# Optimization experiments

Measured on AMD Instinct MI355X. Metric: run time of the kernel, lower is better.

## Reference

```python
import jax
import jax.numpy as jnp
from jax import lax
import numpy as np

TS = 7
DATA_DIM = 1024
HIDDEN = 1024
BATCH = 1024


def setup_inputs() -> dict:
    key = jax.random.key(0)
    ks = jax.random.split(key, 8)
    s = 1.0 / np.sqrt(HIDDEN)
    return {
        "x": jax.random.normal(ks[0], (BATCH, TS, DATA_DIM), dtype=jnp.float32),
        "x_shift": jax.random.normal(ks[1], (BATCH, TS, DATA_DIM), dtype=jnp.float32),
        # PyTorch LSTM params, gate order (i, f, g, o), uniform(-1/sqrt(H), 1/sqrt(H))
        "W_ih": jax.random.uniform(ks[2], (4 * HIDDEN, DATA_DIM), jnp.float32, -s, s),
        "W_hh": jax.random.uniform(ks[3], (4 * HIDDEN, HIDDEN), jnp.float32, -s, s),
        "b_ih": jax.random.uniform(ks[4], (4 * HIDDEN,), jnp.float32, -s, s),
        "b_hh": jax.random.uniform(ks[5], (4 * HIDDEN,), jnp.float32, -s, s),
        "attn_W": jax.random.uniform(ks[6], (1, HIDDEN), jnp.float32, -s, s),
        "attn_b": jax.random.uniform(ks[7], (1,), jnp.float32, -s, s),
    }


def _lstm(x, W_ih, W_hh, b_ih, b_hh):
    # x: [B, T, D] -> h: [B, T, H]; PyTorch gate order i, f, g, o
    B, T, D = x.shape
    H = W_hh.shape[1]
    x_gates = jnp.einsum("btd,gd->btg", x, W_ih) + b_ih + b_hh  # [B, T, 4H]

    def step(carry, xg):
        h, c = carry
        g = xg + h @ W_hh.T  # [B, 4H]
        i, f, gg, o = jnp.split(g, 4, axis=-1)
        i = jax.nn.sigmoid(i)
        f = jax.nn.sigmoid(f)
        gg = jnp.tanh(gg)
        o = jax.nn.sigmoid(o)
        c = f * c + i * gg
        h = o * jnp.tanh(c)
        return (h, c), h

    h0 = jnp.zeros((B, H), x.dtype)
    c0 = jnp.zeros((B, H), x.dtype)
    (_, _), hs = lax.scan(step, (h0, c0), jnp.swapaxes(x_gates, 0, 1))
    return jnp.swapaxes(hs, 0, 1)  # [B, T, H]


def _dam_forward(x, x_shift, W_ih, W_hh, b_ih, b_hh, attn_W, attn_b):
    ts = x.shape[1]
    data_dim = x.shape[2]
    # Temporal covariance: original does bmm -> eye mask -> max(dim=1),
    # which equals relu(diag) since off-diagonal entries become exact zeros.
    t1 = x - x.mean(axis=2, keepdims=True)
    t2 = x_shift - x_shift.mean(axis=2, keepdims=True)
    cov_temp = jnp.maximum(jnp.sum(t1 * t2, axis=2) / ts, 0.0)  # [B, ts]
    # Channel covariance: same trick on [B, data_dim, data_dim] diagonal.
    c1 = x - x.mean(axis=1, keepdims=True)
    c2 = x_shift - x_shift.mean(axis=1, keepdims=True)
    cov_channel = jnp.maximum(jnp.sum(c1 * c2, axis=1) / data_dim, 0.0)  # [B, data_dim]
    # Outer product -> [B, ts, data_dim]
    dist = cov_temp[:, :, None] * cov_channel[:, None, :]
    h = _lstm(dist, W_ih, W_hh, b_ih, b_hh)  # [B, ts, H]
    spatial_attn = jax.nn.softmax(h, axis=1)
    h_tanh = jnp.tanh(h)
    temporal_attn = jax.nn.sigmoid(h_tanh @ attn_W.T + attn_b)  # [B, ts, 1]
    return spatial_attn, temporal_attn


def reference(x, x_shift, W_ih, W_hh, b_ih, b_hh, attn_W, attn_b):
    return _dam_forward(x, x_shift, W_ih, W_hh, b_ih, b_hh, attn_W, attn_b)
```

## Files before the change

kernel.cpp:

```cpp
#include <hip/hip_runtime.h>
#include <math.h>

#define BSZ 1024
#define TS 7
#define DD 1024
#define HH 1024
#define NG 4096

typedef _Float16 f16x8 __attribute__((ext_vector_type(8)));
typedef _Float16 f16x4 __attribute__((ext_vector_type(4)));
typedef float f32x4 __attribute__((ext_vector_type(4)));

__device__ __forceinline__ float sigm_(float x) { return 1.f / (1.f + __expf(-x)); }
__device__ __forceinline__ float tanh_(float x) { return 1.f - 2.f / (__expf(2.f * x) + 1.f); }

__device__ __forceinline__ void gload16(const _Float16* g, _Float16* l) {
  __builtin_amdgcn_global_load_lds(
      (const __attribute__((address_space(1))) void*)g,
      (__attribute__((address_space(3))) void*)l, 16, 0, 0);
}

__global__ __launch_bounds__(256) void conv_w(const float* __restrict__ wih,
                                              const float* __restrict__ whh,
                                              _Float16* __restrict__ o_ih,
                                              _Float16* __restrict__ o_hh) {
  const int N4 = NG * DD / 4;
  for (int i = blockIdx.x * 256 + threadIdx.x; i < 2 * N4;
       i += gridDim.x * 256) {
    const float4 v = (i < N4) ? ((const float4*)wih)[i] : ((const float4*)whh)[i - N4];
    f16x4 o;
    o[0] = (_Float16)v.x; o[1] = (_Float16)v.y;
    o[2] = (_Float16)v.z; o[3] = (_Float16)v.w;
    if (i < N4) ((f16x4*)o_ih)[i] = o;
    else        ((f16x4*)o_hh)[i - N4] = o;
  }
}

__global__ __launch_bounds__(256) void cov_kernel(
    const float* __restrict__ x, const float* __restrict__ xsh,
    float* __restrict__ covT, _Float16* __restrict__ covC16) {
  const int b = blockIdx.x, tid = threadIdx.x;
  const float4* xb = (const float4*)(x + (size_t)b * TS * DD);
  const float4* yb = (const float4*)(xsh + (size_t)b * TS * DD);
  float4 xv[TS], yv[TS];
#pragma unroll
  for (int t = 0; t < TS; t++) {
    xv[t] = xb[t * 256 + tid];
    yv[t] = yb[t * 256 + tid];
  }
  f16x4 cc;
#pragma unroll
  for (int q = 0; q < 4; q++) {
    float sx = 0.f, sy = 0.f, sxy = 0.f;
#pragma unroll
    for (int t = 0; t < TS; t++) {
      float a = ((const float*)&xv[t])[q];
      float c = ((const float*)&yv[t])[q];
      sx += a; sy += c; sxy += a * c;
    }
    float v = (sxy - sx * sy * (1.f / TS)) * (1.f / DD);
    cc[q] = (_Float16)(v > 0.f ? v : 0.f);
  }
  *(f16x4*)&covC16[(size_t)b * DD + tid * 4] = cc;

  float psx[TS], psy[TS], psxy[TS];
#pragma unroll
  for (int t = 0; t < TS; t++) {
    float4 a = xv[t], c = yv[t];
    psx[t] = a.x + a.y + a.z + a.w;
    psy[t] = c.x + c.y + c.z + c.w;
    psxy[t] = a.x * c.x + a.y * c.y + a.z * c.z + a.w * c.w;
  }
#pragma unroll
  for (int t = 0; t < TS; t++) {
    for (int m = 32; m >= 1; m >>= 1) {
      psx[t] += __shfl_xor(psx[t], m);
      psy[t] += __shfl_xor(psy[t], m);
      psxy[t] += __shfl_xor(psxy[t], m);
    }
  }
  __shared__ float red[3][4][TS];
  const int wave = tid >> 6, lane = tid & 63;
  if (lane == 0) {
#pragma unroll
    for (int t = 0; t < TS; t++) {
      red[0][wave][t] = psx[t];
      red[1][wave][t] = psy[t];
      red[2][wave][t] = psxy[t];
    }
  }
  __syncthreads();
  if (tid < TS) {
    float sx = red[0][0][tid] + red[0][1][tid] + red[0][2][tid] + red[0][3][tid];
    float sy = red[1][0][tid] + red[1][1][tid] + red[1][2][tid] + red[1][3][tid];
    float sxy = red[2][0][tid] + red[2][1][tid] + red[2][2][tid] + red[2][3][tid];
    float v = (sxy - sx * sy * (1.f / DD)) * (1.f / TS);
    covT[b * TS + tid] = v > 0.f ? v : 0.f;
  }
}

template <int MODE>
__global__ __launch_bounds__(256) void fused_step(
    const _Float16* __restrict__ A, int lda, const _Float16* __restrict__ W,
    const float* __restrict__ covT, int t, _Float16* __restrict__ M16,
    const float* __restrict__ b_ih, const float* __restrict__ b_hh,
    float* __restrict__ cbuf, _Float16* __restrict__ hout)
{
  __shared__ __align__(16) char smem[49152];
  _Float16* As0 = (_Float16*)smem;
  _Float16* Bs0 = (_Float16*)(smem + 8192);
  _Float16* As1 = (_Float16*)(smem + 24576);
  _Float16* Bs1 = (_Float16*)(smem + 32768);
  float* gls = (float*)smem;

  const int tid = threadIdx.x;
  const int wave = tid >> 6, lane = tid & 63;
  const int l15 = lane & 15, lhi = lane >> 4;
  const int rowBase = blockIdx.y * 64;
  const int jBase = blockIdx.x * 32;
  const int sRow = tid >> 3;
  const int sColSw = (((tid & 7) ^ (sRow & 7)) * 8);
  const int ldsOff = (tid & ~63) * 8;

  f32x4 acc[4][2] = {};

#define STAGE(as, bs, kt)                                                     \
  {                                                                           \
    const int k0 = (kt)*64;                                                   \
    gload16(&A[(size_t)(rowBase + sRow) * lda + k0 + sColSw], (as) + ldsOff); \
    gload16(&A[(size_t)(rowBase + 32 + sRow) * lda + k0 + sColSw],            \
            (as) + 2048 + ldsOff);                                            \
    gload16(&W[(size_t)(0 * HH + jBase + sRow) * DD + k0 + sColSw],           \
            (bs) + 0 + ldsOff);                                               \
    gload16(&W[(size_t)(1 * HH + jBase + sRow) * DD + k0 + sColSw],           \
            (bs) + 2048 + ldsOff);                                            \
    gload16(&W[(size_t)(2 * HH + jBase + sRow) * DD + k0 + sColSw],           \
            (bs) + 4096 + ldsOff);                                            \
    gload16(&W[(size_t)(3 * HH + jBase + sRow) * DD + k0 + sColSw],           \
            (bs) + 6144 + ldsOff);                                            \
  }

#define COMPUTE(as, bs)                                                       \
  {                                                                           \
    _Pragma("unroll") for (int kk = 0; kk < 2; ++kk) {                        \
      const int akx = (kk * 32 + lhi * 8) ^ ((l15 & 7) << 3);                 \
      f16x8 af[4], bf[2];                                                     \
      _Pragma("unroll") for (int mf = 0; mf < 4; ++mf) af[mf] =               \
          *(const f16x8*)&(as)[(mf * 16 + l15) * 64 + akx];                   \
      _Pragma("unroll") for (int nf = 0; nf < 2; ++nf) bf[nf] =               \
          *(const f16x8*)&(bs)[(wave * 32 + nf * 16 + l15) * 64 + akx];       \
      _Pragma("unroll") for (int mf = 0; mf < 4; ++mf)                        \
          _Pragma("unroll") for (int nf = 0; nf < 2; ++nf) acc[mf][nf] =      \
              __builtin_amdgcn_mfma_f32_16x16x32_f16(af[mf], bf[nf],          \
                                                     acc[mf][nf], 0, 0, 0);   \
    }                                                                         \
  }

  STAGE(As0, Bs0, 0);
  __syncthreads();
#pragma unroll
  for (int kt = 0; kt < 16; kt += 2) {
    STAGE(As1, Bs1, kt + 1);
    COMPUTE(As0, Bs0);
    __syncthreads();
    if (kt + 2 < 16) STAGE(As0, Bs0, kt + 2);
    COMPUTE(As1, Bs1);
    __syncthreads();
  }

#pragma unroll
  for (int mf = 0; mf < 4; ++mf)
#pragma unroll
    for (int nf = 0; nf < 2; ++nf)
#pragma unroll
      for (int r = 0; r < 4; ++r)
        gls[(wave * 64 + mf * 16 + lhi * 4 + r) * 33 + nf * 16 + l15] =
            acc[mf][nf][r];
  __syncthreads();

  const int jj = tid & 31;
  const int j = jBase + jj;
  float bia[4];
#pragma unroll
  for (int g = 0; g < 4; ++g) bia[g] = b_ih[g * HH + j] + b_hh[g * HH + j];

#pragma unroll
  for (int k = 0; k < 8; ++k) {
    const int row = k * 8 + (tid >> 5);
    const int b = rowBase + row;
    const float a = covT[b * TS + t];
    float pre[4];
#pragma unroll
    for (int g = 0; g < 4; ++g) {
      const float gv = gls[(g * 64 + row) * 33 + jj];
      if (MODE == 0) {
        M16[(size_t)b * NG + g * HH + j] = (_Float16)gv;
        pre[g] = a * gv + bia[g];
      } else {
        pre[g] = gv + a * (float)M16[(size_t)b * NG + g * HH + j] + bia[g];
      }
    }
    const float i_ = sigm_(pre[0]), f_ = sigm_(pre[1]);
    const float g_ = tanh_(pre[2]), o_ = sigm_(pre[3]);
    const float c_ =
        (MODE == 1 ? f_ * cbuf[(size_t)b * HH + j] : 0.f) + i_ * g_;
    cbuf[(size_t)b * HH + j] = c_;
    hout[(size_t)b * TS * HH + j] = (_Float16)(o_ * tanh_(c_));
  }
#undef STAGE
#undef COMPUTE
}

__global__ __launch_bounds__(256) void finale(
    const _Float16* __restrict__ h16, const float* __restrict__ attn_W,
    const float* __restrict__ attn_b, float* __restrict__ out) {
  const int b = blockIdx.x, tid = threadIdx.x;
  const f16x4* hb = (const f16x4*)(h16 + (size_t)b * TS * HH);
  float v[TS][4];
#pragma unroll
  for (int t = 0; t < TS; t++) {
    f16x4 hv = hb[t * 256 + tid];
#pragma unroll
    for (int q = 0; q < 4; q++) v[t][q] = (float)hv[q];
  }
  const float4 aw = ((const float4*)attn_W)[tid];
  const float awa[4] = {aw.x, aw.y, aw.z, aw.w};

  float4 outv[TS];
#pragma unroll
  for (int q = 0; q < 4; q++) {
    float m = -1e30f;
#pragma unroll
    for (int t = 0; t < TS; t++) m = fmaxf(m, v[t][q]);
    float e[TS], s = 0.f;
#pragma unroll
    for (int t = 0; t < TS; t++) {
      e[t] = __expf(v[t][q] - m);
      s += e[t];
    }
    const float inv = 1.f / s;
#pragma unroll
    for (int t = 0; t < TS; t++) ((float*)&outv[t])[q] = e[t] * inv;
  }
#pragma unroll
  for (int t = 0; t < TS; t++)
    ((float4*)out)[(size_t)b * TS * 256 + t * 256 + tid] = outv[t];

  float pt[TS];
#pragma unroll
  for (int t = 0; t < TS; t++) {
    pt[t] = tanh_(v[t][0]) * awa[0] + tanh_(v[t][1]) * awa[1] +
            tanh_(v[t][2]) * awa[2] + tanh_(v[t][3]) * awa[3];
  }
#pragma unroll
  for (int t = 0; t < TS; t++)
    for (int m = 32; m >= 1; m >>= 1) pt[t] += __shfl_xor(pt[t], m);
  __shared__ float red[4][TS];
  const int wave = tid >> 6, lane = tid & 63;
  if (lane == 0) {
#pragma unroll
    for (int t = 0; t < TS; t++) red[wave][t] = pt[t];
  }
  __syncthreads();
  if (tid < TS) {
    float s = red[0][tid] + red[1][tid] + red[2][tid] + red[3][tid];
    out[(size_t)BSZ * TS * HH + b * TS + tid] = sigm_(s + attn_b[0]);
  }
}

extern "C" void kernel_launch(void* const* d_in, const int* in_sizes, int n_in,
                              void* d_out, int out_size, void* d_ws,
                              size_t ws_size, hipStream_t stream) {
  const float* x = (const float*)d_in[0];
  const float* xsh = (const float*)d_in[1];
  const float* W_ih = (const float*)d_in[2];
  const float* W_hh = (const float*)d_in[3];
  const float* b_ih = (const float*)d_in[4];
  const float* b_hh = (const float*)d_in[5];
  const float* attn_W = (const float*)d_in[6];
  const float* attn_b = (const float*)d_in[7];
  float* out = (float*)d_out;
  float* w = (float*)d_ws;

  float* covT = w;
  _Float16* covC16 = (_Float16*)(w + 8192);
  _Float16* Wih16 = (_Float16*)(w + 532480);
  _Float16* Whh16 = (_Float16*)(w + 2629632);
  _Float16* M16 = (_Float16*)(w + 4726784);
  float* cbuf = w + 6823936;
  _Float16* h16 = (_Float16*)(w + 7872512);

  conv_w<<<1024, 256, 0, stream>>>(W_ih, W_hh, Wih16, Whh16);
  cov_kernel<<<dim3(BSZ), dim3(256), 0, stream>>>(x, xsh, covT, covC16);

  fused_step<0><<<dim3(32, 16), dim3(256), 0, stream>>>(
      covC16, DD, Wih16, covT, 0, M16, b_ih, b_hh, cbuf, h16);
  for (int t = 1; t < TS; t++) {
    fused_step<1><<<dim3(32, 16), dim3(256), 0, stream>>>(
        h16 + (size_t)(t - 1) * HH, TS * HH, Whh16, covT, t, M16, b_ih, b_hh,
        cbuf, h16 + (size_t)t * HH);
  }
  finale<<<dim3(BSZ), dim3(256), 0, stream>>>(h16, attn_W, attn_b, out);
}
```

Before: 255.2 us.

## Replace per-timestep LSTM launches with persistent kernel using grid barriers

```diff
diff --git a/kernel.cpp b/kernel.cpp
--- a/kernel.cpp
+++ b/kernel.cpp
@@ -6,6 +6,7 @@
 #define DD 1024
 #define HH 1024
 #define NG 4096
+#define NBLK 512
 
 typedef _Float16 f16x8 __attribute__((ext_vector_type(8)));
 typedef _Float16 f16x4 __attribute__((ext_vector_type(4)));
@@ -18,6 +19,18 @@
   __builtin_amdgcn_global_load_lds(
       (const __attribute__((address_space(1))) void*)g,
       (__attribute__((address_space(3))) void*)l, 16, 0, 0);
+}
+
+__device__ __forceinline__ void grid_barrier(unsigned* c) {
+  __threadfence();
+  __syncthreads();
+  if (threadIdx.x == 0) {
+    __hip_atomic_fetch_add(c, 1u, __ATOMIC_ACQ_REL, __HIP_MEMORY_SCOPE_AGENT);
+    while (__hip_atomic_load(c, __ATOMIC_ACQUIRE, __HIP_MEMORY_SCOPE_AGENT) <
+           (unsigned)NBLK) {
+    }
+  }
+  __syncthreads();
 }
 
 __global__ __launch_bounds__(256) void conv_w(const float* __restrict__ wih,
@@ -99,19 +112,15 @@
   }
 }
 
-template <int MODE>
-__global__ __launch_bounds__(256) void fused_step(
-    const _Float16* __restrict__ A, int lda, const _Float16* __restrict__ W,
-    const float* __restrict__ covT, int t, _Float16* __restrict__ M16,
+__global__ __launch_bounds__(256, 2) void persist_lstm(
+    const _Float16* __restrict__ covC16, const _Float16* __restrict__ Wih,
+    const _Float16* __restrict__ Whh, const float* __restrict__ covT,
     const float* __restrict__ b_ih, const float* __restrict__ b_hh,
-    float* __restrict__ cbuf, _Float16* __restrict__ hout)
-{
-  __shared__ __align__(16) char smem[49152];
-  _Float16* As0 = (_Float16*)smem;
-  _Float16* Bs0 = (_Float16*)(smem + 8192);
-  _Float16* As1 = (_Float16*)(smem + 24576);
-  _Float16* Bs1 = (_Float16*)(smem + 32768);
-  float* gls = (float*)smem;
+    _Float16* __restrict__ h16, unsigned* __restrict__ cnt) {
+  __shared__ __align__(16) _Float16 As0[64 * 64];
+  __shared__ __align__(16) _Float16 Bs0[128 * 64];
+  __shared__ __align__(16) _Float16 As1[64 * 64];
+  __shared__ __align__(16) _Float16 Bs1[128 * 64];
 
   const int tid = threadIdx.x;
   const int wave = tid >> 6, lane = tid & 63;
@@ -122,90 +131,94 @@
   const int sColSw = (((tid & 7) ^ (sRow & 7)) * 8);
   const int ldsOff = (tid & ~63) * 8;
 
-  f32x4 acc[4][2] = {};
-
-#define STAGE(as, bs, kt)                                                     \
-  {                                                                           \
-    const int k0 = (kt)*64;                                                   \
-    gload16(&A[(size_t)(rowBase + sRow) * lda + k0 + sColSw], (as) + ldsOff); \
-    gload16(&A[(size_t)(rowBase + 32 + sRow) * lda + k0 + sColSw],            \
-            (as) + 2048 + ldsOff);                                            \
-    gload16(&W[(size_t)(0 * HH + jBase + sRow) * DD + k0 + sColSw],           \
-            (bs) + 0 + ldsOff);                                               \
-    gload16(&W[(size_t)(1 * HH + jBase + sRow) * DD + k0 + sColSw],           \
-            (bs) + 2048 + ldsOff);                                            \
-    gload16(&W[(size_t)(2 * HH + jBase + sRow) * DD + k0 + sColSw],           \
-            (bs) + 4096 + ldsOff);                                            \
-    gload16(&W[(size_t)(3 * HH + jBase + sRow) * DD + k0 + sColSw],           \
-            (bs) + 6144 + ldsOff);                                            \
-  }
-
-#define COMPUTE(as, bs)                                                       \
-  {                                                                           \
-    _Pragma("unroll") for (int kk = 0; kk < 2; ++kk) {                        \
-      const int akx = (kk * 32 + lhi * 8) ^ ((l15 & 7) << 3);                 \
-      f16x8 af[4], bf[2];                                                     \
-      _Pragma("unroll") for (int mf = 0; mf < 4; ++mf) af[mf] =               \
-          *(const f16x8*)&(as)[(mf * 16 + l15) * 64 + akx];                   \
-      _Pragma("unroll") for (int nf = 0; nf < 2; ++nf) bf[nf] =               \
-          *(const f16x8*)&(bs)[(wave * 32 + nf * 16 + l15) * 64 + akx];       \
-      _Pragma("unroll") for (int mf = 0; mf < 4; ++mf)                        \
-          _Pragma("unroll") for (int nf = 0; nf < 2; ++nf) acc[mf][nf] =      \
-              __builtin_amdgcn_mfma_f32_16x16x32_f16(af[mf], bf[nf],          \
-                                                     acc[mf][nf], 0, 0, 0);   \
-    }                                                                         \
-  }
-
-  STAGE(As0, Bs0, 0);
-  __syncthreads();
-#pragma unroll
-  for (int kt = 0; kt < 16; kt += 2) {
-    STAGE(As1, Bs1, kt + 1);
-    COMPUTE(As0, Bs0);
+  float bia[4][2];
+#pragma unroll
+  for (int g = 0; g < 4; ++g)
+#pragma unroll
+    for (int js = 0; js < 2; ++js) {
+      const int j = jBase + l15 + js * 16;
+      bia[g][js] = b_ih[g * HH + j] + b_hh[g * HH + j];
+    }
+
+  f32x4 Mreg[8];
+  float cst[2][4];
+
+#define STAGE(as, bs, kt)                                                      \
+  {                                                                            \
+    const int k0 = (kt)*64;                                                    \
+    gload16(&Ap[(size_t)(rowBase + sRow) * ldap + k0 + sColSw], (as) + ldsOff);\
+    gload16(&Ap[(size_t)(rowBase + 32 + sRow) * ldap + k0 + sColSw],           \
+            (as) + 2048 + ldsOff);                                             \
+    gload16(&Wp[(size_t)(0 * HH + jBase + sRow) * DD + k0 + sColSw],           \
+            (bs) + 0 + ldsOff);                                                \
+    gload16(&Wp[(size_t)(1 * HH + jBase + sRow) * DD + k0 + sColSw],           \
+            (bs) + 2048 + ldsOff);                                             \
+    gload16(&Wp[(size_t)(2 * HH + jBase + sRow) * DD + k0 + sColSw],           \
+            (bs) + 4096 + ldsOff);                                             \
+    gload16(&Wp[(size_t)(3 * HH + jBase + sRow) * DD + k0 + sColSw],           \
+            (bs) + 6144 + ldsOff);                                             \
+  }
+
+#define COMPUTE(as, bs)                                                        \
+  {                                                                            \
+    _Pragma("unroll") for (int kk = 0; kk < 2; ++kk) {                         \
+      const int akx = (kk * 32 + lhi * 8) ^ ((l15 & 7) << 3);                  \
+      const f16x8 af = *(const f16x8*)&(as)[(wave * 16 + l15) * 64 + akx];     \
+      _Pragma("unroll") for (int nf = 0; nf < 8; ++nf) {                       \
+        const f16x8 bf = *(const f16x8*)&(bs)[(nf * 16 + l15) * 64 + akx];     \
+        acc[nf] = __builtin_amdgcn_mfma_f32_16x16x32_f16(af, bf, acc[nf],      \
+                                                         0, 0, 0);             \
+      }                                                                        \
+    }                                                                          \
+  }
+
+#pragma unroll 1
+  for (int t = 0; t < TS; ++t) {
+    const _Float16* Ap = t ? h16 + (size_t)(t - 1) * HH : covC16;
+    const int ldap = t ? TS * HH : DD;
+    const _Float16* Wp = t ? Whh : Wih;
+    f32x4 acc[8] = {};
+
+    STAGE(As0, Bs0, 0);
     __syncthreads();
-    if (kt + 2 < 16) STAGE(As0, Bs0, kt + 2);
-    COMPUTE(As1, Bs1);
-    __syncthreads();
-  }
-
-#pragma unroll
-  for (int mf = 0; mf < 4; ++mf)
-#pragma unroll
-    for (int nf = 0; nf < 2; ++nf)
-#pragma unroll
-      for (int r = 0; r < 4; ++r)
-        gls[(wave * 64 + mf * 16 + lhi * 4 + r) * 33 + nf * 16 + l15] =
-            acc[mf][nf][r];
-  __syncthreads();
-
-  const int jj = tid & 31;
-  const int j = jBase + jj;
-  float bia[4];
-#pragma unroll
-  for (int g = 0; g < 4; ++g) bia[g] = b_ih[g * HH + j] + b_hh[g * HH + j];
-
-#pragma unroll
-  for (int k = 0; k < 8; ++k) {
-    const int row = k * 8 + (tid >> 5);
-    const int b = rowBase + row;
-    const float a = covT[b * TS + t];
-    float pre[4];
-#pragma unroll
-    for (int g = 0; g < 4; ++g) {
-      const float gv = gls[(g * 64 + row) * 33 + jj];
-      if (MODE == 0) {
-        M16[(size_t)b * NG + g * HH + j] = (_Float16)gv;
-        pre[g] = a * gv + bia[g];
-      } else {
-        pre[g] = gv + a * (float)M16[(size_t)b * NG + g * HH + j] + bia[g];
+    for (int kt = 0; kt < 16; kt += 2) {
+      STAGE(As1, Bs1, kt + 1);
+      COMPUTE(As0, Bs0);
+      __syncthreads();
+      if (kt + 2 < 16) STAGE(As0, Bs0, kt + 2);
+      COMPUTE(As1, Bs1);
+      __syncthreads();
+    }
+
+    float covt[4];
+#pragma unroll
+    for (int r = 0; r < 4; ++r)
+      covt[r] = covT[(size_t)(rowBase + wave * 16 + lhi * 4 + r) * TS + t];
+#pragma unroll
+    for (int js = 0; js < 2; ++js)
+#pragma unroll
+      for (int r = 0; r < 4; ++r) {
+        float pre[4];
+#pragma unroll
+        for (int g = 0; g < 4; ++g) {
+          const int nf = g * 2 + js;
+          if (t == 0) {
+            Mreg[nf][r] = acc[nf][r];
+            pre[g] = covt[r] * acc[nf][r] + bia[g][js];
+          } else {
+            pre[g] = acc[nf][r] + covt[r] * Mreg[nf][r] + bia[g][js];
+          }
+        }
+        const float i_ = sigm_(pre[0]), f_ = sigm_(pre[1]);
+        const float g_ = tanh_(pre[2]), o_ = sigm_(pre[3]);
+        const float c_ = (t ? f_ * cst[js][r] : 0.f) + i_ * g_;
+        cst[js][r] = c_;
+        const size_t row = rowBase + wave * 16 + lhi * 4 + r;
+        h16[row * TS * HH + (size_t)t * HH + jBase + l15 + js * 16] =
+            (_Float16)(o_ * tanh_(c_));
       }
-    }
-    const float i_ = sigm_(pre[0]), f_ = sigm_(pre[1]);
-    const float g_ = tanh_(pre[2]), o_ = sigm_(pre[3]);
-    const float c_ =
-        (MODE == 1 ? f_ * cbuf[(size_t)b * HH + j] : 0.f) + i_ * g_;
-    cbuf[(size_t)b * HH + j] = c_;
-    hout[(size_t)b * TS * HH + j] = (_Float16)(o_ * tanh_(c_));
+
+    if (t < TS - 1) grid_barrier(&cnt[t]);
   }
 #undef STAGE
 #undef COMPUTE
@@ -282,23 +295,17 @@
   float* out = (float*)d_out;
   float* w = (float*)d_ws;
 
-  float* covT = w;
+  unsigned* cnt = (unsigned*)w;
+  float* covT = w + 16;
   _Float16* covC16 = (_Float16*)(w + 8192);
   _Float16* Wih16 = (_Float16*)(w + 532480);
   _Float16* Whh16 = (_Float16*)(w + 2629632);
-  _Float16* M16 = (_Float16*)(w + 4726784);
-  float* cbuf = w + 6823936;
-  _Float16* h16 = (_Float16*)(w + 7872512);
-
+  _Float16* h16 = (_Float16*)(w + 4726784);
+
+  hipMemsetAsync(cnt, 0, 64, stream);
   conv_w<<<1024, 256, 0, stream>>>(W_ih, W_hh, Wih16, Whh16);
   cov_kernel<<<dim3(BSZ), dim3(256), 0, stream>>>(x, xsh, covT, covC16);
-
-  fused_step<0><<<dim3(32, 16), dim3(256), 0, stream>>>(
-      covC16, DD, Wih16, covT, 0, M16, b_ih, b_hh, cbuf, h16);
-  for (int t = 1; t < TS; t++) {
-    fused_step<1><<<dim3(32, 16), dim3(256), 0, stream>>>(
-        h16 + (size_t)(t - 1) * HH, TS * HH, Whh16, covT, t, M16, b_ih, b_hh,
-        cbuf, h16 + (size_t)t * HH);
-  }
+  persist_lstm<<<dim3(32, 16), dim3(256), 0, stream>>>(
+      covC16, Wih16, Whh16, covT, b_ih, b_hh, h16, cnt);
   finale<<<dim3(BSZ), dim3(256), 0, stream>>>(h16, attn_W, attn_b, out);
 }
```

Result: slower. 629.4 us (+146.7%).
